# Performance work log

Measured on AMD Instinct MI355X. Metric: run time of the kernel, lower is better.

The kernel has to match this reference:

```python
import jax, jax.numpy as jnp
import numpy as np

EPS_F = 1e-12
M, N = 64, 4096  # feature dim m, num nodes n


def setup_inputs() -> dict:
    key = jax.random.key(0)
    k1, k2, k3, k4 = jax.random.split(key, 4)
    # X: (m, n) node features transposed, as in the repo (features.t())
    X = jax.random.normal(k1, (M, N), dtype=jnp.float32)
    # F: (m, m) parameter, xavier_uniform init
    bound = float(np.sqrt(6.0 / (M + M)))
    F = jax.random.uniform(k2, (M, M), minval=-bound, maxval=bound, dtype=jnp.float32)
    # Q_S: (n, n) orthogonal eigenvector matrix of the (symmetric, normalized) adjacency
    A = jax.random.normal(k3, (N, N), dtype=jnp.float32)
    Q_S, _ = jnp.linalg.qr(A)
    Q_S = Q_S.astype(jnp.float32)
    # Lambda_S: (n, 1) eigenvalues of normalized adjacency, inside (-1, 1)
    Lambda_S = jnp.sort(
        jax.random.uniform(k4, (N, 1), minval=-0.95, maxval=0.95, dtype=jnp.float32), axis=0
    )
    gamma = jnp.asarray(0.8, dtype=jnp.float32)
    return {"X": X, "F": F, "Q_S": Q_S, "Lambda_S": Lambda_S, "gamma": gamma}


def reference(X, F, Q_S, Lambda_S, gamma):
    # g(F) = F^T F / (||F^T F||_F + eps)  -- Frobenius-normalized Gram matrix
    FF = F.T @ F                                   # (m, m)
    G_F = FF / (jnp.linalg.norm(FF) + EPS_F)       # (m, m), symmetric PSD, ||.||_F ~ 1
    # spectral decomposition of g(F)
    Lambda_F, Q_F = jnp.linalg.eigh(G_F)           # (m,), (m, m)
    # closed-form equilibrium of Z = gamma * g(F) Z S^T + X in the joint eigenbasis
    D = 1.0 / (1.0 - gamma * Lambda_F[:, None] * Lambda_S.reshape(1, -1))  # (m, n)
    Z = Q_F @ (D * (Q_F.T @ X @ Q_S)) @ Q_S.T      # (m, n)
    return Z
```

## Files before the change

kernel.cpp:

```cpp
#include <hip/hip_runtime.h>
#include <math.h>


typedef short short8 __attribute__((ext_vector_type(8)));
typedef float floatx16 __attribute__((ext_vector_type(16)));

#define KSPLIT 32
#define KCHUNK 128
constexpr int Mdim = 64;
constexpr int Ndim = 4096;

__device__ inline ushort f2bf(float f) {
    uint u = __float_as_uint(f);
    u += 0x7fff + ((u >> 16) & 1);
    return (ushort)(u >> 16);
}
__device__ inline float bf2f(ushort h) { return __uint_as_float(((uint)h) << 16); }

__device__ inline floatx16 mfma_bf16(short8 a, short8 b, floatx16 c) {
    return __builtin_amdgcn_mfma_f32_32x32x16_bf16(a, b, c, 0, 0, 0);
}

struct SharedGemm { ushort Ah[4096], Al[4096], Bh[4096]; };

__device__ inline void barrier_nodrain() {
    asm volatile("s_waitcnt lgkmcnt(0)" ::: "memory");
    __builtin_amdgcn_s_barrier();
    __builtin_amdgcn_sched_barrier(0);
}

__global__ __launch_bounds__(256) void init_kernel(float* __restrict__ W, float* __restrict__ Z) {
    const int i = blockIdx.x * 256 + threadIdx.x;
    float4 z = {0.f, 0.f, 0.f, 0.f};
    if (i < 65536) *(float4*)&W[i * 4] = z;
    else *(float4*)&Z[(i - 65536) * 4] = z;
}

__device__ void prep_body(SharedGemm& sg, const float* __restrict__ F, float* __restrict__ Gout) {
    const int t = threadIdx.x;
    const int l = t & 63, w = t >> 6;
    const int tm = w & 1, tn = w >> 1;
    const int am = tm * 32 + (l & 31);
    const int bn = tn * 32 + (l & 31);
    const int lk = l >> 5;
    float* red = (float*)sg.Bh;

    {
        const int r = t >> 2, c0 = (t & 3) * 16;
#pragma unroll
        for (int q = 0; q < 4; ++q) {
            float4 v = *(const float4*)&F[r * 64 + c0 + 4 * q];
            float fa[4] = {v.x, v.y, v.z, v.w};
#pragma unroll
            for (int i = 0; i < 4; ++i) {
                int c = c0 + 4 * q + i;
                ushort h = f2bf(fa[i]);
                int idx = c * 64 + (((r >> 3) ^ (c & 7)) * 8) + (r & 7);
                sg.Ah[idx] = h;
                sg.Al[idx] = f2bf(fa[i] - bf2f(h));
            }
        }
    }
    __syncthreads();
    floatx16 acc;
    for (int i = 0; i < 16; ++i) acc[i] = 0.f;
    for (int s16 = 0; s16 < 4; ++s16) {
        int gk = 2 * s16 + lk;
        int ai = am * 64 + ((gk ^ (am & 7)) * 8);
        int bi = bn * 64 + ((gk ^ (bn & 7)) * 8);
        short8 ah = *(const short8*)&sg.Ah[ai];
        short8 al = *(const short8*)&sg.Al[ai];
        short8 bh = *(const short8*)&sg.Ah[bi];
        short8 bl = *(const short8*)&sg.Al[bi];
        acc = mfma_bf16(ah, bh, acc);
        acc = mfma_bf16(al, bh, acc);
        acc = mfma_bf16(ah, bl, acc);
    }
    float ss = 0.f;
    for (int r = 0; r < 16; ++r) ss += acc[r] * acc[r];
    red[t] = ss;
    __syncthreads();
    for (int off = 128; off > 0; off >>= 1) {
        if (t < off) red[t] += red[t + off];
        __syncthreads();
    }
    const float inv = 1.0f / (sqrtf(red[0]) + 1e-12f);
    for (int r = 0; r < 16; ++r) {
        int row = (r & 3) + 8 * (r >> 2) + 4 * lk + tm * 32;
        int col = tn * 32 + (l & 31);
        float v = acc[r] * inv;
        Gout[row * 64 + col] = v;
        ushort h = f2bf(v);
        int idx = row * 64 + (((col >> 3) ^ (row & 7)) * 8 + (col & 7));
        sg.Ah[idx] = h;
        sg.Al[idx] = f2bf(v - bf2f(h));
    }
    for (int j = 1; j < 5; ++j) {
        __syncthreads();
        floatx16 a2;
        for (int i = 0; i < 16; ++i) a2[i] = 0.f;
        for (int s16 = 0; s16 < 4; ++s16) {
            int gk = 2 * s16 + lk;
            int ai = am * 64 + ((gk ^ (am & 7)) * 8);
            int bi = bn * 64 + ((gk ^ (bn & 7)) * 8);
            short8 ah = *(const short8*)&sg.Ah[ai];
            short8 al = *(const short8*)&sg.Al[ai];
            short8 bh = *(const short8*)&sg.Ah[bi];
            short8 bl = *(const short8*)&sg.Al[bi];
            a2 = mfma_bf16(ah, bh, a2);
            a2 = mfma_bf16(al, bh, a2);
            a2 = mfma_bf16(ah, bl, a2);
        }
        __syncthreads();
        for (int r = 0; r < 16; ++r) {
            int row = (r & 3) + 8 * (r >> 2) + 4 * lk + tm * 32;
            int col = tn * 32 + (l & 31);
            float v = a2[r];
            Gout[j * 4096 + row * 64 + col] = v;
            ushort h = f2bf(v);
            int idx = row * 64 + (((col >> 3) ^ (row & 7)) * 8 + (col & 7));
            sg.Ah[idx] = h;
            sg.Al[idx] = f2bf(v - bf2f(h));
        }
    }
}

template <bool TB, bool DOPREP>
__global__ __launch_bounds__(256, 6) void gemm_kernel(const float* __restrict__ A,
                                                      const float* __restrict__ Bm,
                                                      float* __restrict__ C,
                                                      const float* __restrict__ F,
                                                      float* __restrict__ Gp) {
    __shared__ SharedGemm sh;
    const int bid = blockIdx.x;
    if (DOPREP) {
        if (bid == 0) { prep_body(sh, F, Gp); return; }
    }
    const int b = DOPREP ? bid - 1 : bid;
    const int n0 = (b & 63) * 64;
    const int kb = (b >> 6) * KCHUNK;
    const int t = threadIdx.x;
    const int l = t & 63, w = t >> 6;
    const int tm = w & 1, tn = w >> 1;
    const int am = tm * 32 + (l & 31);
    const int bn = tn * 32 + (l & 31);
    const int lk = l >> 5;
    const int sr = t >> 2, sj = t & 3;
    const int nq = t & 15, kr2 = 2 * (t >> 4);

    floatx16 acc;
    for (int i = 0; i < 16; ++i) acc[i] = 0.f;

    float4 bbuf[2][4];
    if (TB) {
#pragma unroll
        for (int s = 0; s < 4; ++s)
            bbuf[0][s] = *(const float4*)&Bm[(size_t)(n0 + sr) * 4096 + kb + 4 * sj + 16 * s];
    } else {
#pragma unroll
        for (int s = 0; s < 2; ++s) {
            bbuf[0][2 * s + 0] = *(const float4*)&Bm[(size_t)(kb + kr2 + 32 * s) * 4096 + n0 + 4 * nq];
            bbuf[0][2 * s + 1] = *(const float4*)&Bm[(size_t)(kb + kr2 + 1 + 32 * s) * 4096 + n0 + 4 * nq];
        }
    }

#pragma unroll
    for (int step = 0; step < KCHUNK / 64; ++step) {
        const int k0 = kb + step * 64;
        const int cur = step & 1, nxt = cur ^ 1;
        float4 av[4];
#pragma unroll
        for (int s = 0; s < 4; ++s)
            av[s] = *(const float4*)&A[sr * 4096 + k0 + 4 * sj + 16 * s];
        if (step + 1 < KCHUNK / 64) {
            const int k1 = k0 + 64;
            if (TB) {
#pragma unroll
                for (int s = 0; s < 4; ++s)
                    bbuf[nxt][s] = *(const float4*)&Bm[(size_t)(n0 + sr) * 4096 + k1 + 4 * sj + 16 * s];
            } else {
#pragma unroll
                for (int s = 0; s < 2; ++s) {
                    bbuf[nxt][2 * s + 0] = *(const float4*)&Bm[(size_t)(k1 + kr2 + 32 * s) * 4096 + n0 + 4 * nq];
                    bbuf[nxt][2 * s + 1] = *(const float4*)&Bm[(size_t)(k1 + kr2 + 1 + 32 * s) * 4096 + n0 + 4 * nq];
                }
            }
        }
        barrier_nodrain();
        if (TB) {
#pragma unroll
            for (int s = 0; s < 4; ++s) {
                int off = 4 * sj + 16 * s;
                int idx = sr * 64 + (((off >> 3) ^ (sr & 7)) * 8 + (off & 7));
                float fb[4] = {bbuf[cur][s].x, bbuf[cur][s].y, bbuf[cur][s].z, bbuf[cur][s].w};
                ushort4 h4;
                ushort* hp = (ushort*)&h4;
#pragma unroll
                for (int i = 0; i < 4; ++i) hp[i] = f2bf(fb[i]);
                *(ushort4*)&sh.Bh[idx] = h4;
            }
        } else {
#pragma unroll
            for (int s = 0; s < 2; ++s) {
                int k = kr2 + 32 * s;
                float fa[4] = {bbuf[cur][2 * s].x, bbuf[cur][2 * s].y, bbuf[cur][2 * s].z, bbuf[cur][2 * s].w};
                float fb[4] = {bbuf[cur][2 * s + 1].x, bbuf[cur][2 * s + 1].y, bbuf[cur][2 * s + 1].z, bbuf[cur][2 * s + 1].w};
#pragma unroll
                for (int i = 0; i < 4; ++i) {
                    int n = 4 * nq + i;
                    int idx = n * 64 + (((k >> 3) ^ (n & 7)) * 8 + (k & 7));
                    ushort2 hp2;
                    hp2.x = f2bf(fa[i]);
                    hp2.y = f2bf(fb[i]);
                    *(ushort2*)&sh.Bh[idx] = hp2;
                }
            }
        }
#pragma unroll
        for (int s = 0; s < 4; ++s) {
            int off = 4 * sj + 16 * s;
            int idx = sr * 64 + (((off >> 3) ^ (sr & 7)) * 8 + (off & 7));
            float fa[4] = {av[s].x, av[s].y, av[s].z, av[s].w};
            ushort4 h4, l4;
            ushort* hp = (ushort*)&h4; ushort* lp = (ushort*)&l4;
#pragma unroll
            for (int i = 0; i < 4; ++i) {
                ushort h = f2bf(fa[i]);
                hp[i] = h; lp[i] = f2bf(fa[i] - bf2f(h));
            }
            *(ushort4*)&sh.Ah[idx] = h4;
            *(ushort4*)&sh.Al[idx] = l4;
        }
        barrier_nodrain();
#pragma unroll
        for (int s16 = 0; s16 < 4; ++s16) {
            int gk = 2 * s16 + lk;
            int ai = am * 64 + ((gk ^ (am & 7)) * 8);
            int bi = bn * 64 + ((gk ^ (bn & 7)) * 8);
            short8 ah = *(const short8*)&sh.Ah[ai];
            short8 al = *(const short8*)&sh.Al[ai];
            short8 bh = *(const short8*)&sh.Bh[bi];
            acc = mfma_bf16(ah, bh, acc);
            acc = mfma_bf16(al, bh, acc);
        }
    }
    const int colg = n0 + tn * 32 + (l & 31);
#pragma unroll
    for (int r = 0; r < 16; ++r) {
        int row = (r & 3) + 8 * (r >> 2) + 4 * lk + tm * 32;
        atomicAdd(&C[row * 4096 + colg], acc[r]);
    }
}

__global__ __launch_bounds__(256) void solve_kernel(const float* __restrict__ W,
                                                    const float* __restrict__ Gp,
                                                    const float* __restrict__ lam,
                                                    const float* __restrict__ gammap,
                                                    float* __restrict__ Y) {
    __shared__ float Gs[64][68];
    __shared__ float T[64][17];
    const int t = threadIdx.x;
    const int c0 = blockIdx.x * 16;
    for (int e = t; e < 1024; e += 256)
        T[e >> 4][e & 15] = W[(e >> 4) * 4096 + c0 + (e & 15)];
    const int tx = t & 15;
    const int r4 = (t >> 4) * 4;
    const float a = gammap[0] * lam[c0 + tx];
    float s = a;
    for (int j = 0; j < 5; ++j) {
        __syncthreads();
        for (int e = t; e < 4096; e += 256) Gs[e >> 6][e & 63] = Gp[j * 4096 + e];
        __syncthreads();
        float u0 = 0.f, u1 = 0.f, u2 = 0.f, u3 = 0.f;
#pragma unroll 8
        for (int k = 0; k < 64; ++k) {
            const float tv = T[k][tx];
            const float4 g = *(const float4*)&Gs[k][r4];
            u0 += g.x * tv; u1 += g.y * tv; u2 += g.z * tv; u3 += g.w * tv;
        }
        __syncthreads();
        T[r4 + 0][tx] += s * u0;
        T[r4 + 1][tx] += s * u1;
        T[r4 + 2][tx] += s * u2;
        T[r4 + 3][tx] += s * u3;
        s = s * s;
    }
    __syncthreads();
    for (int e = t; e < 1024; e += 256)
        Y[(e >> 4) * 4096 + c0 + (e & 15)] = T[e >> 4][e & 15];
}

extern "C" void kernel_launch(void* const* d_in, const int* in_sizes, int n_in,
                              void* d_out, int out_size, void* d_ws, size_t ws_size,
                              hipStream_t stream) {
    const float* X     = (const float*)d_in[0];
    const float* F     = (const float*)d_in[1];
    const float* Qs    = (const float*)d_in[2];
    const float* lam   = (const float*)d_in[3];
    const float* gamma = (const float*)d_in[4];
    float* Z = (float*)d_out;

    float* W  = (float*)d_ws;
    float* Y  = W + Mdim * Ndim;
    float* Gp = Y + Mdim * Ndim;

    init_kernel<<<512, 256, 0, stream>>>(W, Z);
    gemm_kernel<false, true><<<64 * KSPLIT + 1, 256, 0, stream>>>(X, Qs, W, F, Gp);
    solve_kernel<<<Ndim / 16, 256, 0, stream>>>(W, Gp, lam, gamma, Y);
    gemm_kernel<true, false><<<64 * KSPLIT, 256, 0, stream>>>(Y, Qs, Z, nullptr, nullptr);
}
```

Before: 173.4 us.

## Replace atomic split-K accumulation with partial buffers and a reduce kernel

The split-K GEMMs now write per-split partial tiles into a workspace instead of atomically adding into the output. A separate reduce kernel sums the partials, which also removes the zero-init kernel. The split count is halved with a longer K chunk per block, B loads are prefetched two steps ahead, and the occupancy hint is lowered. This trades atomic contention for extra global traffic to write and reread 16 partial tiles, plus two extra launches.

```diff
diff --git a/kernel.cpp b/kernel.cpp
--- a/kernel.cpp
+++ b/kernel.cpp
@@ -5,10 +5,11 @@
 typedef short short8 __attribute__((ext_vector_type(8)));
 typedef float floatx16 __attribute__((ext_vector_type(16)));
 
-#define KSPLIT 32
-#define KCHUNK 128
+#define KSPLIT 16
+#define KCHUNK 256
 constexpr int Mdim = 64;
 constexpr int Ndim = 4096;
+constexpr int TILE = Mdim * Ndim;
 
 __device__ inline ushort f2bf(float f) {
     uint u = __float_as_uint(f);
@@ -27,13 +28,6 @@
     asm volatile("s_waitcnt lgkmcnt(0)" ::: "memory");
     __builtin_amdgcn_s_barrier();
     __builtin_amdgcn_sched_barrier(0);
-}
-
-__global__ __launch_bounds__(256) void init_kernel(float* __restrict__ W, float* __restrict__ Z) {
-    const int i = blockIdx.x * 256 + threadIdx.x;
-    float4 z = {0.f, 0.f, 0.f, 0.f};
-    if (i < 65536) *(float4*)&W[i * 4] = z;
-    else *(float4*)&Z[(i - 65536) * 4] = z;
 }
 
 __device__ void prep_body(SharedGemm& sg, const float* __restrict__ F, float* __restrict__ Gout) {
@@ -125,8 +119,24 @@
     }
 }
 
+template <bool TB>
+__device__ inline void load_b(float4 (&dst)[4], const float* __restrict__ Bm,
+                              int n0, int kk, int sr, int sj, int nq, int kr2) {
+    if constexpr (TB) {
+#pragma unroll
+        for (int s = 0; s < 4; ++s)
+            dst[s] = *(const float4*)&Bm[(size_t)(n0 + sr) * 4096 + kk + 4 * sj + 16 * s];
+    } else {
+#pragma unroll
+        for (int s = 0; s < 2; ++s) {
+            dst[2 * s + 0] = *(const float4*)&Bm[(size_t)(kk + kr2 + 32 * s) * 4096 + n0 + 4 * nq];
+            dst[2 * s + 1] = *(const float4*)&Bm[(size_t)(kk + kr2 + 1 + 32 * s) * 4096 + n0 + 4 * nq];
+        }
+    }
+}
+
 template <bool TB, bool DOPREP>
-__global__ __launch_bounds__(256, 6) void gemm_kernel(const float* __restrict__ A,
+__global__ __launch_bounds__(256, 4) void gemm_kernel(const float* __restrict__ A,
                                                       const float* __restrict__ Bm,
                                                       float* __restrict__ C,
                                                       const float* __restrict__ F,
@@ -138,7 +148,8 @@
     }
     const int b = DOPREP ? bid - 1 : bid;
     const int n0 = (b & 63) * 64;
-    const int kb = (b >> 6) * KCHUNK;
+    const int ks = b >> 6;
+    const int kb = ks * KCHUNK;
     const int t = threadIdx.x;
     const int l = t & 63, w = t >> 6;
     const int tm = w & 1, tn = w >> 1;
@@ -151,48 +162,26 @@
     floatx16 acc;
     for (int i = 0; i < 16; ++i) acc[i] = 0.f;
 
-    float4 bbuf[2][4];
-    if (TB) {
-#pragma unroll
-        for (int s = 0; s < 4; ++s)
-            bbuf[0][s] = *(const float4*)&Bm[(size_t)(n0 + sr) * 4096 + kb + 4 * sj + 16 * s];
-    } else {
-#pragma unroll
-        for (int s = 0; s < 2; ++s) {
-            bbuf[0][2 * s + 0] = *(const float4*)&Bm[(size_t)(kb + kr2 + 32 * s) * 4096 + n0 + 4 * nq];
-            bbuf[0][2 * s + 1] = *(const float4*)&Bm[(size_t)(kb + kr2 + 1 + 32 * s) * 4096 + n0 + 4 * nq];
-        }
-    }
+    float4 bbuf[4][4];
+    load_b<TB>(bbuf[0], Bm, n0, kb, sr, sj, nq, kr2);
+    load_b<TB>(bbuf[1], Bm, n0, kb + 64, sr, sj, nq, kr2);
 
 #pragma unroll
     for (int step = 0; step < KCHUNK / 64; ++step) {
         const int k0 = kb + step * 64;
-        const int cur = step & 1, nxt = cur ^ 1;
         float4 av[4];
 #pragma unroll
         for (int s = 0; s < 4; ++s)
             av[s] = *(const float4*)&A[sr * 4096 + k0 + 4 * sj + 16 * s];
-        if (step + 1 < KCHUNK / 64) {
-            const int k1 = k0 + 64;
-            if (TB) {
-#pragma unroll
-                for (int s = 0; s < 4; ++s)
-                    bbuf[nxt][s] = *(const float4*)&Bm[(size_t)(n0 + sr) * 4096 + k1 + 4 * sj + 16 * s];
-            } else {
-#pragma unroll
-                for (int s = 0; s < 2; ++s) {
-                    bbuf[nxt][2 * s + 0] = *(const float4*)&Bm[(size_t)(k1 + kr2 + 32 * s) * 4096 + n0 + 4 * nq];
-                    bbuf[nxt][2 * s + 1] = *(const float4*)&Bm[(size_t)(k1 + kr2 + 1 + 32 * s) * 4096 + n0 + 4 * nq];
-                }
-            }
-        }
+        if (step + 2 < KCHUNK / 64)
+            load_b<TB>(bbuf[step + 2], Bm, n0, k0 + 128, sr, sj, nq, kr2);
         barrier_nodrain();
         if (TB) {
 #pragma unroll
             for (int s = 0; s < 4; ++s) {
                 int off = 4 * sj + 16 * s;
                 int idx = sr * 64 + (((off >> 3) ^ (sr & 7)) * 8 + (off & 7));
-                float fb[4] = {bbuf[cur][s].x, bbuf[cur][s].y, bbuf[cur][s].z, bbuf[cur][s].w};
+                float fb[4] = {bbuf[step][s].x, bbuf[step][s].y, bbuf[step][s].z, bbuf[step][s].w};
                 ushort4 h4;
                 ushort* hp = (ushort*)&h4;
 #pragma unroll
@@ -203,8 +192,8 @@
 #pragma unroll
             for (int s = 0; s < 2; ++s) {
                 int k = kr2 + 32 * s;
-                float fa[4] = {bbuf[cur][2 * s].x, bbuf[cur][2 * s].y, bbuf[cur][2 * s].z, bbuf[cur][2 * s].w};
-                float fb[4] = {bbuf[cur][2 * s + 1].x, bbuf[cur][2 * s + 1].y, bbuf[cur][2 * s + 1].z, bbuf[cur][2 * s + 1].w};
+                float fa[4] = {bbuf[step][2 * s].x, bbuf[step][2 * s].y, bbuf[step][2 * s].z, bbuf[step][2 * s].w};
+                float fb[4] = {bbuf[step][2 * s + 1].x, bbuf[step][2 * s + 1].y, bbuf[step][2 * s + 1].z, bbuf[step][2 * s + 1].w};
 #pragma unroll
                 for (int i = 0; i < 4; ++i) {
                     int n = 4 * nq + i;
@@ -244,12 +233,25 @@
             acc = mfma_bf16(al, bh, acc);
         }
     }
+    float* Cp = C + (size_t)ks * TILE;
     const int colg = n0 + tn * 32 + (l & 31);
 #pragma unroll
     for (int r = 0; r < 16; ++r) {
         int row = (r & 3) + 8 * (r >> 2) + 4 * lk + tm * 32;
-        atomicAdd(&C[row * 4096 + colg], acc[r]);
-    }
+        Cp[row * 4096 + colg] = acc[r];
+    }
+}
+
+__global__ __launch_bounds__(256) void reduce_kernel(const float* __restrict__ P,
+                                                     float* __restrict__ out) {
+    const int i = blockIdx.x * 256 + threadIdx.x;
+    float4 a = {0.f, 0.f, 0.f, 0.f};
+#pragma unroll
+    for (int s = 0; s < KSPLIT; ++s) {
+        const float4 v = *(const float4*)&P[(size_t)s * TILE + 4 * i];
+        a.x += v.x; a.y += v.y; a.z += v.z; a.w += v.w;
+    }
+    *(float4*)&out[4 * i] = a;
 }
 
 __global__ __launch_bounds__(256) void solve_kernel(const float* __restrict__ W,
@@ -300,12 +302,14 @@
     const float* gamma = (const float*)d_in[4];
     float* Z = (float*)d_out;
 
-    float* W  = (float*)d_ws;
-    float* Y  = W + Mdim * Ndim;
-    float* Gp = Y + Mdim * Ndim;
-
-    init_kernel<<<512, 256, 0, stream>>>(W, Z);
-    gemm_kernel<false, true><<<64 * KSPLIT + 1, 256, 0, stream>>>(X, Qs, W, F, Gp);
+    float* P  = (float*)d_ws;
+    float* W  = P + (size_t)KSPLIT * TILE;
+    float* Y  = W + TILE;
+    float* Gp = Y + TILE;
+
+    gemm_kernel<false, true><<<64 * KSPLIT + 1, 256, 0, stream>>>(X, Qs, P, F, Gp);
+    reduce_kernel<<<256, 256, 0, stream>>>(P, W);
     solve_kernel<<<Ndim / 16, 256, 0, stream>>>(W, Gp, lam, gamma, Y);
-    gemm_kernel<true, false><<<64 * KSPLIT, 256, 0, stream>>>(Y, Qs, Z, nullptr, nullptr);
-}
+    gemm_kernel<true, false><<<64 * KSPLIT, 256, 0, stream>>>(Y, Qs, P, nullptr, nullptr);
+    reduce_kernel<<<256, 256, 0, stream>>>(P, Z);
+}
```

Measured after the change: 155.4 us. -10.3%, faster.
